# Performance work log

Hardware: AMD Instinct MI355X
Metric: run time of the kernel (lower is better)

## Reference

```python
import jax, jax.numpy as jnp
import numpy as np

CTX = 768   # ctx_len in the original module
C = 768     # n_embd
B = 16
T = 768
K_EPS = 1e-8


def setup_inputs() -> dict:
    key = jax.random.key(0)
    ks = jax.random.split(key, 10)
    scale = 1.0 / np.sqrt(C)
    x = jax.random.normal(ks[0], (B, T, C), jnp.float32)
    time_decay = jax.random.normal(ks[1], (C, 1), jnp.float32) * 0.1
    time_first = jnp.full((C, 1), np.log(0.3), jnp.float32)
    time_mix_k = jax.random.uniform(ks[2], (1, 1, C), jnp.float32)
    time_mix_v = jax.random.uniform(ks[3], (1, 1, C), jnp.float32)
    time_mix_r = jax.random.uniform(ks[4], (1, 1, C), jnp.float32)
    Wk = jax.random.normal(ks[5], (C, C), jnp.float32) * scale
    Wv = jax.random.normal(ks[6], (C, C), jnp.float32) * scale
    Wr = jax.random.normal(ks[7], (C, C), jnp.float32) * scale
    Wo = jax.random.normal(ks[8], (C, C), jnp.float32) * scale
    return {"x": x, "time_decay": time_decay, "time_first": time_first,
            "time_mix_k": time_mix_k, "time_mix_v": time_mix_v, "time_mix_r": time_mix_r,
            "Wk": Wk, "Wv": Wv, "Wr": Wr, "Wo": Wo}


def reference(x, time_decay, time_first, time_mix_k, time_mix_v, time_mix_r, Wk, Wv, Wr, Wo):
    Bb, Tt, Cc = x.shape
    # time_shift: xx[t] = x[t-1], xx[0] = 0
    xx = jnp.pad(x, ((0, 0), (1, 0), (0, 0)))[:, :Tt]
    xk = x * time_mix_k + xx * (1.0 - time_mix_k)
    xv = x * time_mix_v + xx * (1.0 - time_mix_v)
    xr = x * time_mix_r + xx * (1.0 - time_mix_r)
    # projections (nn.Linear, no bias: y = x @ W.T); k, v laid out [B, C, T]
    k = jnp.einsum('btc,oc->bot', xk, Wk)
    v = jnp.einsum('btc,oc->bot', xv, Wv)
    r = jnp.einsum('btc,oc->bto', xr, Wr)
    k = jnp.exp(jnp.minimum(k, 60.0))
    kv = k * v
    # decay kernel: time_w = cat([exp(time_decay)*time_curve, time_first]); w = exp(time_w)[:, -T:]
    curve = (jnp.arange(CTX - 1) - (CTX - 2)).astype(x.dtype)  # [-(CTX-2) .. 0]
    tw = jnp.concatenate([jnp.exp(time_decay) * curve[None, :], time_first], axis=-1)  # [C, CTX]
    w = jnp.exp(tw)[:, -Tt:]            # [C, T]
    kern = w[:, None, :]                # [C, 1, T] depthwise kernel

    def causal_conv(z):  # z: [B, C, T] -> [B, C, T], left-padded cross-correlation
        return jax.lax.conv_general_dilated(
            z, kern, window_strides=(1,), padding=[(Tt - 1, 0)],
            feature_group_count=Cc, dimension_numbers=('NCH', 'OIH', 'NCH'))

    wkv = causal_conv(kv)
    wk = causal_conv(k) + K_EPS
    rwkv = jax.nn.sigmoid(r) * jnp.transpose(wkv / wk, (0, 2, 1))  # [B, T, C]
    return jnp.einsum('btc,oc->bto', rwkv, Wo)
```

## Files before the change

kernel.cpp:

```cpp
#include <hip/hip_runtime.h>
#include <math.h>

#define Mq 12288
#define Nq 768
#define Kq 768
#define Tq 768
#define Bq 16
#define Cq 768
#define BK 64
#define BM 128

typedef __bf16 bf16x8 __attribute__((ext_vector_type(8)));
typedef __bf16 bf16x4 __attribute__((ext_vector_type(4)));
typedef __bf16 bf16x2 __attribute__((ext_vector_type(2)));
typedef float  floatx4 __attribute__((ext_vector_type(4)));

#define GLD_LDS16(g, l) __builtin_amdgcn_global_load_lds(                      \
    (const __attribute__((address_space(1))) unsigned int*)(g),                \
    (__attribute__((address_space(3))) unsigned int*)(l), 16, 0, 0)

__global__ __launch_bounds__(256)
void prep_kernel(const float* __restrict__ x,
                 const float* __restrict__ mk, const float* __restrict__ mv,
                 const float* __restrict__ mr,
                 const float* __restrict__ Wk, const float* __restrict__ Wv,
                 const float* __restrict__ Wr, const float* __restrict__ Wo,
                 __bf16* __restrict__ xk, __bf16* __restrict__ xv,
                 __bf16* __restrict__ xr, __bf16* __restrict__ wp)
{
    const int bid = blockIdx.x;
    if (bid < 4608) {
        const int i  = bid * 256 + threadIdx.x;
        const int c8 = i % (Cq / 8);
        const int m  = i / (Cq / 8);
        const int t  = m % Tq;
        const int c0 = c8 * 8;

        const float4 xa = *(const float4*)(x + (size_t)m * Cq + c0);
        const float4 xb = *(const float4*)(x + (size_t)m * Cq + c0 + 4);
        float4 pa = make_float4(0.f, 0.f, 0.f, 0.f);
        float4 pb = make_float4(0.f, 0.f, 0.f, 0.f);
        if (t > 0) {
            pa = *(const float4*)(x + (size_t)(m - 1) * Cq + c0);
            pb = *(const float4*)(x + (size_t)(m - 1) * Cq + c0 + 4);
        }
        const float xc[8] = { xa.x, xa.y, xa.z, xa.w, xb.x, xb.y, xb.z, xb.w };
        const float xp[8] = { pa.x, pa.y, pa.z, pa.w, pb.x, pb.y, pb.z, pb.w };

        const size_t o = (size_t)m * Cq + c0;
        {
            const float4 ma = *(const float4*)(mk + c0);
            const float4 mb = *(const float4*)(mk + c0 + 4);
            const float mm[8] = { ma.x, ma.y, ma.z, ma.w, mb.x, mb.y, mb.z, mb.w };
            bf16x8 ov;
#pragma unroll
            for (int j = 0; j < 8; ++j)
                ov[j] = (__bf16)fmaf(mm[j], xc[j] - xp[j], xp[j]);
            *(bf16x8*)(xk + o) = ov;
        }
        {
            const float4 ma = *(const float4*)(mv + c0);
            const float4 mb = *(const float4*)(mv + c0 + 4);
            const float mm[8] = { ma.x, ma.y, ma.z, ma.w, mb.x, mb.y, mb.z, mb.w };
            bf16x8 ov;
#pragma unroll
            for (int j = 0; j < 8; ++j)
                ov[j] = (__bf16)fmaf(mm[j], xc[j] - xp[j], xp[j]);
            *(bf16x8*)(xv + o) = ov;
        }
        {
            const float4 ma = *(const float4*)(mr + c0);
            const float4 mb = *(const float4*)(mr + c0 + 4);
            const float mm[8] = { ma.x, ma.y, ma.z, ma.w, mb.x, mb.y, mb.z, mb.w };
            bf16x8 ov;
#pragma unroll
            for (int j = 0; j < 8; ++j)
                ov[j] = (__bf16)fmaf(mm[j], xc[j] - xp[j], xp[j]);
            *(bf16x8*)(xr + o) = ov;
        }
    } else {
        const int i   = (bid - 4608) * 256 + threadIdx.x;
        const int a   = i / 73728;
        const int off = (i - a * 73728) * 8;
        const float* s = (a == 0) ? Wk : (a == 1) ? Wv : (a == 2) ? Wr : Wo;
        const float4 va = *(const float4*)(s + off);
        const float4 vb = *(const float4*)(s + off + 4);
        bf16x8 r = { (__bf16)va.x, (__bf16)va.y, (__bf16)va.z, (__bf16)va.w,
                     (__bf16)vb.x, (__bf16)vb.y, (__bf16)vb.z, (__bf16)vb.w };
        *(bf16x8*)(wp + (size_t)a * 589824 + off) = r;
    }
}

template<bool KVR>
__global__ __launch_bounds__(256, 3)
void mfma_gemm(const __bf16* __restrict__ A0, const __bf16* __restrict__ A1,
               const __bf16* __restrict__ A2,
               const __bf16* __restrict__ W,
               __bf16* __restrict__ OUTb, float* __restrict__ OUTf)
{
    __shared__ __bf16 As[BM * BK];
    __shared__ __bf16 Bs[128 * BK];

    const int STRIPS = KVR ? 18 : 6;

    const int i_    = blockIdx.x;
    const int xcd   = i_ & 7;
    const int j_    = i_ >> 3;
    const int strip = j_ % STRIPS;
    const int mt    = xcd * 12 + j_ / STRIPS;

    const int tid   = threadIdx.x;
    const int wave  = tid >> 6;
    const int lane  = tid & 63;
    const int m0    = mt * BM;
    const int matid = KVR ? strip / 6 : 0;
    const int n0    = KVR ? (strip % 6) * 128 : strip * 128;
    const int wn0   = strip * 128;

    const __bf16* A = KVR ? (matid == 0 ? A0 : matid == 1 ? A1 : A2) : A0;

    const int r8 = lane >> 3;
    const int sc = (lane & 7) ^ r8;
    const __bf16* gA[4];  __bf16* lA[4];
    const __bf16* gB[4];  __bf16* lB[4];
#pragma unroll
    for (int i = 0; i < 4; ++i) {
        const int row = (wave * 4 + i) * 8 + r8;
        gA[i] = A + (size_t)(m0 + row) * Kq + sc * 8;
        lA[i] = As + (wave * 4 + i) * 512;
        gB[i] = W + (size_t)(wn0 + row) * Kq + sc * 8;
        lB[i] = Bs + (wave * 4 + i) * 512;
    }

    const int wm   = wave & 1;
    const int wn   = wave >> 1;
    const int xRow = wm * 64 + (lane & 15);
    const int wRow = wn * 64 + (lane & 15);
    const int lk   = lane >> 4;

    floatx4 acc[4][4];
#pragma unroll
    for (int i = 0; i < 4; ++i)
#pragma unroll
        for (int j = 0; j < 4; ++j) acc[i][j] = (floatx4){0.f, 0.f, 0.f, 0.f};

    for (int kt = 0; kt < Kq / BK; ++kt) {
#pragma unroll
        for (int i = 0; i < 4; ++i) { GLD_LDS16(gA[i], lA[i]); gA[i] += BK; }
#pragma unroll
        for (int i = 0; i < 4; ++i) { GLD_LDS16(gB[i], lB[i]); gB[i] += BK; }
        __syncthreads();

#pragma unroll
        for (int kk = 0; kk < 2; ++kk) {
            bf16x8 wF[4], xF[4];
#pragma unroll
            for (int i = 0; i < 4; ++i) {
                const int r = wRow + i * 16;
                wF[i] = *(const bf16x8*)(Bs + r * BK +
                                         (((kk << 2) | lk) ^ (r & 7)) * 8);
            }
#pragma unroll
            for (int j = 0; j < 4; ++j) {
                const int r = xRow + j * 16;
                xF[j] = *(const bf16x8*)(As + r * BK +
                                         (((kk << 2) | lk) ^ (r & 7)) * 8);
            }
#pragma unroll
            for (int i = 0; i < 4; ++i)
#pragma unroll
                for (int j = 0; j < 4; ++j)
                    acc[i][j] = __builtin_amdgcn_mfma_f32_16x16x32_bf16(
                        wF[i], xF[j], acc[i][j], 0, 0, 0);
        }
        __syncthreads();
    }

#pragma unroll
    for (int j = 0; j < 4; ++j) {
        const int tok = m0 + wm * 64 + j * 16 + (lane & 15);
#pragma unroll
        for (int i = 0; i < 4; ++i) {
            const int ch = n0 + wn * 64 + i * 16 + (lane >> 4) * 4;
            if (KVR) {
                float v0 = acc[i][j][0], v1 = acc[i][j][1];
                float v2 = acc[i][j][2], v3 = acc[i][j][3];
                if (matid == 0) {
                    v0 = expf(fminf(v0, 60.f)); v1 = expf(fminf(v1, 60.f));
                    v2 = expf(fminf(v2, 60.f)); v3 = expf(fminf(v3, 60.f));
                } else if (matid == 2) {
                    v0 = 1.f / (1.f + expf(-v0)); v1 = 1.f / (1.f + expf(-v1));
                    v2 = 1.f / (1.f + expf(-v2)); v3 = 1.f / (1.f + expf(-v3));
                }
                bf16x4 o = { (__bf16)v0, (__bf16)v1, (__bf16)v2, (__bf16)v3 };
                *(bf16x4*)(OUTb + (size_t)matid * Mq * Nq +
                           (size_t)tok * Nq + ch) = o;
            } else {
                floatx4 o = acc[i][j];
                *(floatx4*)(OUTf + (size_t)tok * Nq + ch) = o;
            }
        }
    }
}

#define SEG 16
#define SLEN (Tq / SEG)

__global__ __launch_bounds__(1024)
void scan_kernel(const __bf16* __restrict__ kb, const __bf16* __restrict__ vb,
                 __bf16* rb,
                 const float* __restrict__ td, const float* __restrict__ tf)
{
    __shared__ float2 aS[SEG][64];
    __shared__ float2 bS[SEG][64];

    const int cx  = threadIdx.x;
    const int seg = threadIdx.y;
    const int c0  = blockIdx.x * 128 + cx * 2;
    const int b   = blockIdx.y;

    const float d0 = expf(td[c0]),     d1 = expf(td[c0 + 1]);
    const float w0 = expf(-d0),        w1 = expf(-d1);
    const float u0 = expf(tf[c0]),     u1 = expf(tf[c0 + 1]);

    const size_t base = ((size_t)b * Tq + seg * SLEN) * Cq + c0;

    float a0 = 0.f, a1 = 0.f, s0 = 0.f, s1 = 0.f;
#pragma unroll 4
    for (int t = 0; t < SLEN; ++t) {
        const size_t idx = base + (size_t)t * Cq;
        const bf16x2 k2 = *(const bf16x2*)(kb + idx);
        const bf16x2 v2 = *(const bf16x2*)(vb + idx);
        const float k0 = (float)k2[0], k1 = (float)k2[1];
        a0 = fmaf(w0, a0, k0 * (float)v2[0]);
        a1 = fmaf(w1, a1, k1 * (float)v2[1]);
        s0 = fmaf(w0, s0, k0);
        s1 = fmaf(w1, s1, k1);
    }
    aS[seg][cx] = make_float2(a0, a1);
    bS[seg][cx] = make_float2(s0, s1);
    __syncthreads();

    if (seg == 0) {
        const float W0 = expf(-d0 * (float)SLEN);
        const float W1 = expf(-d1 * (float)SLEN);
        float ia0 = 0.f, ia1 = 0.f, ib0 = 0.f, ib1 = 0.f;
#pragma unroll
        for (int s = 0; s < SEG; ++s) {
            const float2 ta = aS[s][cx];
            const float2 tb = bS[s][cx];
            aS[s][cx] = make_float2(ia0, ia1);
            bS[s][cx] = make_float2(ib0, ib1);
            ia0 = fmaf(W0, ia0, ta.x);  ia1 = fmaf(W1, ia1, ta.y);
            ib0 = fmaf(W0, ib0, tb.x);  ib1 = fmaf(W1, ib1, tb.y);
        }
    }
    __syncthreads();

    const float2 ain = aS[seg][cx];
    const float2 bin = bS[seg][cx];
    a0 = ain.x; a1 = ain.y; s0 = bin.x; s1 = bin.y;
#pragma unroll 2
    for (int t = 0; t < SLEN; ++t) {
        const size_t idx = base + (size_t)t * Cq;
        const bf16x2 k2 = *(const bf16x2*)(kb + idx);
        const bf16x2 v2 = *(const bf16x2*)(vb + idx);
        const bf16x2 r2 = *(const bf16x2*)(rb + idx);
        const float k0 = (float)k2[0], k1 = (float)k2[1];
        const float kv0 = k0 * (float)v2[0], kv1 = k1 * (float)v2[1];
        const float n0 = fmaf(u0, kv0, a0), n1 = fmaf(u1, kv1, a1);
        const float e0 = fmaf(u0, k0, s0) + 1e-8f;
        const float e1 = fmaf(u1, k1, s1) + 1e-8f;
        const float i0 = __builtin_amdgcn_rcpf(e0);
        const float i1 = __builtin_amdgcn_rcpf(e1);
        bf16x2 o = { (__bf16)((float)r2[0] * n0 * i0),
                     (__bf16)((float)r2[1] * n1 * i1) };
        *(bf16x2*)(rb + idx) = o;
        a0 = fmaf(w0, a0, kv0);  a1 = fmaf(w1, a1, kv1);
        s0 = fmaf(w0, s0, k0);   s1 = fmaf(w1, s1, k1);
    }
}

extern "C" void kernel_launch(void* const* d_in, const int* in_sizes, int n_in,
                              void* d_out, int out_size, void* d_ws, size_t ws_size,
                              hipStream_t stream)
{
    const float* x  = (const float*)d_in[0];
    const float* td = (const float*)d_in[1];
    const float* tf = (const float*)d_in[2];
    const float* mk = (const float*)d_in[3];
    const float* mv = (const float*)d_in[4];
    const float* mr = (const float*)d_in[5];
    const float* Wk = (const float*)d_in[6];
    const float* Wv = (const float*)d_in[7];
    const float* Wr = (const float*)d_in[8];
    const float* Wo = (const float*)d_in[9];

    const size_t MC = (size_t)Mq * Cq;

    __bf16* xk = (__bf16*)d_out;
    __bf16* xv = xk + MC;

    __bf16* xr   = (__bf16*)d_ws;
    __bf16* kbuf = xr + MC;
    __bf16* vbuf = kbuf + MC;
    __bf16* rbuf = vbuf + MC;
    __bf16* Wp   = rbuf + MC;
    __bf16* Wob  = Wp + 3 * 589824;

    prep_kernel<<<5760, 256, 0, stream>>>(x, mk, mv, mr, Wk, Wv, Wr, Wo,
                                          xk, xv, xr, Wp);

    mfma_gemm<true><<<18 * 96, 256, 0, stream>>>(
        xk, xv, xr, Wp, kbuf, nullptr);

    scan_kernel<<<dim3(Cq / 128, Bq), dim3(64, SEG), 0, stream>>>(
        kbuf, vbuf, rbuf, td, tf);

    mfma_gemm<false><<<6 * 96, 256, 0, stream>>>(
        rbuf, nullptr, nullptr, Wob, nullptr, (float*)d_out);
}
```

Before: 221.1 us.

## Replace KVR projection GEMM with 256x256-tile, 8-wave, double-buffered pipelined kernel

The fused k/v/r projection GEMM moves from 128x128 tiles with 4 waves to 256x256 tiles with 8 waves and 128KB of LDS. Global-to-LDS loads are double-buffered and interleaved with four MFMA quadrant phases, using explicit barriers, vmcnt waits and s_setprio. The aim is to hide load latency and raise data reuse per tile. In exchange, occupancy drops (432 blocks, 2 per CU) and the hand-written wait counts make the schedule fragile. The output GEMM becomes a separate non-templated kernel with unchanged logic.

```diff
diff --git a/kernel.cpp b/kernel.cpp
--- a/kernel.cpp
+++ b/kernel.cpp
@@ -8,6 +8,7 @@
 #define Bq 16
 #define Cq 768
 #define BK 64
+#define NKT (Kq / BK)
 #define BM 128
 
 typedef __bf16 bf16x8 __attribute__((ext_vector_type(8)));
@@ -91,18 +92,168 @@
     }
 }
 
-template<bool KVR>
-__global__ __launch_bounds__(256, 3)
-void mfma_gemm(const __bf16* __restrict__ A0, const __bf16* __restrict__ A1,
+__device__ __forceinline__ void stageW(const __bf16* Wb, __bf16* ldsW,
+                                       int kt, int qc, int wv, int lane)
+{
+    const int sc = (lane & 7) ^ (lane >> 3);
+#pragma unroll
+    for (int g = 0; g < 2; ++g) {
+        const int gi = wv * 2 + g;
+        const int r0 = (gi >> 2) * 64 + qc * 32 + (gi & 3) * 8;
+        GLD_LDS16(Wb + (size_t)(r0 + (lane >> 3)) * Kq + kt * 64 + sc * 8,
+                  ldsW + r0 * 64);
+    }
+}
+__device__ __forceinline__ void stageX(const __bf16* Xb, __bf16* ldsX,
+                                       int kt, int qt, int wv, int lane)
+{
+    const int sc = (lane & 7) ^ (lane >> 3);
+#pragma unroll
+    for (int g = 0; g < 2; ++g) {
+        const int gi = wv * 2 + g;
+        const int r0 = (gi >> 3) * 128 + qt * 64 + (gi & 7) * 8;
+        GLD_LDS16(Xb + (size_t)(r0 + (lane >> 3)) * Kq + kt * 64 + sc * 8,
+                  ldsX + r0 * 64);
+    }
+}
+
+#define PHASE(QC, QT, STAGE_STMT) do {                                         \
+    bf16x8 wF[2][2], xF[4][2];                                                 \
+    _Pragma("unroll")                                                          \
+    for (int ii = 0; ii < 2; ++ii) {                                           \
+        const int r = wn * 64 + QC * 32 + ii * 16 + (lane & 15);               \
+        _Pragma("unroll")                                                      \
+        for (int kk = 0; kk < 2; ++kk)                                         \
+            wF[ii][kk] = *(const bf16x8*)(ldsW + r * 64 +                      \
+                             ((((kk) << 2) | lk) ^ (r & 7)) * 8);              \
+    }                                                                          \
+    _Pragma("unroll")                                                          \
+    for (int jj = 0; jj < 4; ++jj) {                                           \
+        const int r = wm * 128 + QT * 64 + jj * 16 + (lane & 15);              \
+        _Pragma("unroll")                                                      \
+        for (int kk = 0; kk < 2; ++kk)                                         \
+            xF[jj][kk] = *(const bf16x8*)(ldsX + r * 64 +                      \
+                             ((((kk) << 2) | lk) ^ (r & 7)) * 8);              \
+    }                                                                          \
+    STAGE_STMT;                                                                \
+    __builtin_amdgcn_s_barrier();                                              \
+    asm volatile("s_waitcnt lgkmcnt(0)" ::: "memory");                         \
+    __builtin_amdgcn_s_setprio(1);                                             \
+    _Pragma("unroll")                                                          \
+    for (int ii = 0; ii < 2; ++ii)                                             \
+        _Pragma("unroll")                                                      \
+        for (int jj = 0; jj < 4; ++jj)                                         \
+            _Pragma("unroll")                                                  \
+            for (int kk = 0; kk < 2; ++kk)                                     \
+                acc[QC * 2 + ii][QT * 4 + jj] =                                \
+                    __builtin_amdgcn_mfma_f32_16x16x32_bf16(                   \
+                        wF[ii][kk], xF[jj][kk],                                \
+                        acc[QC * 2 + ii][QT * 4 + jj], 0, 0, 0);               \
+    __builtin_amdgcn_s_setprio(0);                                             \
+    __builtin_amdgcn_s_barrier();                                              \
+} while (0)
+
+__global__ __launch_bounds__(512, 2)
+void gemm_kvr8(const __bf16* __restrict__ A0, const __bf16* __restrict__ A1,
                const __bf16* __restrict__ A2,
                const __bf16* __restrict__ W,
-               __bf16* __restrict__ OUTb, float* __restrict__ OUTf)
+               __bf16* __restrict__ OUTb)
+{
+    __shared__ __bf16 LDS[65536];
+
+    const int bid  = blockIdx.x;
+    const int xcd  = bid & 7;
+    const int j_   = bid >> 3;
+    const int nt   = j_ % 9;
+    const int mt   = xcd * 6 + j_ / 9;
+
+    const int tid  = threadIdx.x;
+    const int wv   = tid >> 6;
+    const int lane = tid & 63;
+    const int wm   = wv >> 2;
+    const int wn   = wv & 3;
+    const int lk   = lane >> 4;
+
+    const int m0    = mt * 256;
+    const int matid = nt / 3;
+    const int nc0   = (nt % 3) * 256;
+
+    const __bf16* Xb = (matid == 0) ? A0 : (matid == 1) ? A1 : A2;
+    const __bf16* Wb = W + (size_t)(matid * 768 + nc0) * Kq;
+    Xb += (size_t)m0 * Kq;
+
+    floatx4 acc[4][8];
+#pragma unroll
+    for (int i = 0; i < 4; ++i)
+#pragma unroll
+        for (int j = 0; j < 8; ++j) acc[i][j] = (floatx4){0.f, 0.f, 0.f, 0.f};
+
+#pragma unroll
+    for (int t = 0; t < 2; ++t) {
+        __bf16* lw = LDS + t * 32768;
+        __bf16* lx = lw + 16384;
+        stageX(Xb, lx, t, 0, wv, lane);
+        stageX(Xb, lx, t, 1, wv, lane);
+        stageW(Wb, lw, t, 0, wv, lane);
+        stageW(Wb, lw, t, 1, wv, lane);
+    }
+    asm volatile("s_waitcnt vmcnt(0)" ::: "memory");
+    __builtin_amdgcn_s_barrier();
+
+    for (int u = 0; u < NKT - 1; ++u) {
+        const __bf16* ldsW = LDS + (u & 1) * 32768;
+        const __bf16* ldsX = ldsW + 16384;
+        __bf16* sN = LDS + ((u + 1) & 1) * 32768;
+        __bf16* sC = LDS + (u & 1) * 32768;
+
+        PHASE(0, 0, { if (u >= 1)       stageX(Xb, sN + 16384, u + 1, 1, wv, lane); });
+        PHASE(1, 0, { if (u >= 1)       stageW(Wb, sN,         u + 1, 1, wv, lane); });
+        PHASE(0, 1, { if (u < NKT - 2)  stageX(Xb, sC + 16384, u + 2, 0, wv, lane); });
+        PHASE(1, 1, { if (u < NKT - 2)  stageW(Wb, sC,         u + 2, 0, wv, lane); });
+
+        if (u < NKT - 2) asm volatile("s_waitcnt vmcnt(4)" ::: "memory");
+        else             asm volatile("s_waitcnt vmcnt(0)" ::: "memory");
+        __builtin_amdgcn_s_barrier();
+    }
+    {
+        const __bf16* ldsW = LDS + ((NKT - 1) & 1) * 32768;
+        const __bf16* ldsX = ldsW + 16384;
+        PHASE(0, 0, {});
+        PHASE(1, 0, {});
+        PHASE(0, 1, {});
+        PHASE(1, 1, {});
+    }
+
+#pragma unroll
+    for (int j = 0; j < 8; ++j) {
+        const int tok = m0 + wm * 128 + j * 16 + (lane & 15);
+#pragma unroll
+        for (int i = 0; i < 4; ++i) {
+            const int ch = nc0 + wn * 64 + i * 16 + (lane >> 4) * 4;
+            float v0 = acc[i][j][0], v1 = acc[i][j][1];
+            float v2 = acc[i][j][2], v3 = acc[i][j][3];
+            if (matid == 0) {
+                v0 = expf(fminf(v0, 60.f)); v1 = expf(fminf(v1, 60.f));
+                v2 = expf(fminf(v2, 60.f)); v3 = expf(fminf(v3, 60.f));
+            } else if (matid == 2) {
+                v0 = 1.f / (1.f + expf(-v0)); v1 = 1.f / (1.f + expf(-v1));
+                v2 = 1.f / (1.f + expf(-v2)); v3 = 1.f / (1.f + expf(-v3));
+            }
+            bf16x4 o = { (__bf16)v0, (__bf16)v1, (__bf16)v2, (__bf16)v3 };
+            *(bf16x4*)(OUTb + (size_t)matid * Mq * Nq +
+                       (size_t)tok * Nq + ch) = o;
+        }
+    }
+}
+
+__global__ __launch_bounds__(256, 3)
+void mfma_gemm_o(const __bf16* __restrict__ A0, const __bf16* __restrict__ W,
+                 float* __restrict__ OUTf)
 {
     __shared__ __bf16 As[BM * BK];
     __shared__ __bf16 Bs[128 * BK];
 
-    const int STRIPS = KVR ? 18 : 6;
-
+    const int STRIPS = 6;
     const int i_    = blockIdx.x;
     const int xcd   = i_ & 7;
     const int j_    = i_ >> 3;
@@ -113,11 +264,7 @@
     const int wave  = tid >> 6;
     const int lane  = tid & 63;
     const int m0    = mt * BM;
-    const int matid = KVR ? strip / 6 : 0;
-    const int n0    = KVR ? (strip % 6) * 128 : strip * 128;
-    const int wn0   = strip * 128;
-
-    const __bf16* A = KVR ? (matid == 0 ? A0 : matid == 1 ? A1 : A2) : A0;
+    const int n0    = strip * 128;
 
     const int r8 = lane >> 3;
     const int sc = (lane & 7) ^ r8;
@@ -126,9 +273,9 @@
 #pragma unroll
     for (int i = 0; i < 4; ++i) {
         const int row = (wave * 4 + i) * 8 + r8;
-        gA[i] = A + (size_t)(m0 + row) * Kq + sc * 8;
+        gA[i] = A0 + (size_t)(m0 + row) * Kq + sc * 8;
         lA[i] = As + (wave * 4 + i) * 512;
-        gB[i] = W + (size_t)(wn0 + row) * Kq + sc * 8;
+        gB[i] = W + (size_t)(n0 + row) * Kq + sc * 8;
         lB[i] = Bs + (wave * 4 + i) * 512;
     }
 
@@ -144,7 +291,7 @@
 #pragma unroll
         for (int j = 0; j < 4; ++j) acc[i][j] = (floatx4){0.f, 0.f, 0.f, 0.f};
 
-    for (int kt = 0; kt < Kq / BK; ++kt) {
+    for (int kt = 0; kt < NKT; ++kt) {
 #pragma unroll
         for (int i = 0; i < 4; ++i) { GLD_LDS16(gA[i], lA[i]); gA[i] += BK; }
 #pragma unroll
@@ -182,23 +329,8 @@
 #pragma unroll
         for (int i = 0; i < 4; ++i) {
             const int ch = n0 + wn * 64 + i * 16 + (lane >> 4) * 4;
-            if (KVR) {
-                float v0 = acc[i][j][0], v1 = acc[i][j][1];
-                float v2 = acc[i][j][2], v3 = acc[i][j][3];
-                if (matid == 0) {
-                    v0 = expf(fminf(v0, 60.f)); v1 = expf(fminf(v1, 60.f));
-                    v2 = expf(fminf(v2, 60.f)); v3 = expf(fminf(v3, 60.f));
-                } else if (matid == 2) {
-                    v0 = 1.f / (1.f + expf(-v0)); v1 = 1.f / (1.f + expf(-v1));
-                    v2 = 1.f / (1.f + expf(-v2)); v3 = 1.f / (1.f + expf(-v3));
-                }
-                bf16x4 o = { (__bf16)v0, (__bf16)v1, (__bf16)v2, (__bf16)v3 };
-                *(bf16x4*)(OUTb + (size_t)matid * Mq * Nq +
-                           (size_t)tok * Nq + ch) = o;
-            } else {
-                floatx4 o = acc[i][j];
-                *(floatx4*)(OUTf + (size_t)tok * Nq + ch) = o;
-            }
+            floatx4 o = acc[i][j];
+            *(floatx4*)(OUTf + (size_t)tok * Nq + ch) = o;
         }
     }
 }
@@ -311,12 +443,10 @@
     prep_kernel<<<5760, 256, 0, stream>>>(x, mk, mv, mr, Wk, Wv, Wr, Wo,
                                           xk, xv, xr, Wp);
 
-    mfma_gemm<true><<<18 * 96, 256, 0, stream>>>(
-        xk, xv, xr, Wp, kbuf, nullptr);
+    gemm_kvr8<<<432, 512, 0, stream>>>(xk, xv, xr, Wp, kbuf);
 
     scan_kernel<<<dim3(Cq / 128, Bq), dim3(64, SEG), 0, stream>>>(
         kbuf, vbuf, rbuf, td, tf);
 
-    mfma_gemm<false><<<6 * 96, 256, 0, stream>>>(
-        rbuf, nullptr, nullptr, Wob, nullptr, (float*)d_out);
-}
+    mfma_gemm_o<<<6 * 96, 256, 0, stream>>>(rbuf, Wob, (float*)d_out);
+}
```

After: 233.1 us. 5.4% more time.
